# Optimization experiments

Measured on AMD Instinct MI355X. Metric: run time of the kernel, lower is better.

The kernel has to match this reference:

```python
import jax, jax.numpy as jnp
import numpy as np

D_MODEL = 1024
N_HEADS = 16
D_K = D_MODEL // N_HEADS
B, S = 4, 1024


def setup_inputs() -> dict:
    key = jax.random.key(0)
    ks = jax.random.split(key, 9)
    inp = {
        "q": jax.random.normal(ks[0], (B, S, D_MODEL), jnp.float32),
        "k": jax.random.normal(ks[1], (B, S, D_MODEL), jnp.float32),
        "v": jax.random.normal(ks[2], (B, S, D_MODEL), jnp.float32),
        # causal mask, broadcastable to [B, H, S, S]; 0 => masked
        "mask": jnp.tril(jnp.ones((1, 1, S, S), jnp.int32)),
        # torch nn.Linear weights: y = x @ W.T + b, W is [out, in]
        "Wq": jax.random.normal(ks[3], (D_MODEL, D_MODEL), jnp.float32) * 0.02,
        "bq": jnp.zeros((D_MODEL,), jnp.float32),
        "Wk": jax.random.normal(ks[4], (D_MODEL, D_MODEL), jnp.float32) * 0.02,
        "bk": jnp.zeros((D_MODEL,), jnp.float32),
        "Wv": jax.random.normal(ks[5], (D_MODEL, D_MODEL), jnp.float32) * 0.02,
        "bv": jnp.zeros((D_MODEL,), jnp.float32),
    }
    return inp


def _head_split(x):
    # [B, S, D] -> [B, H, S, d_k]
    b, s, _ = x.shape
    return x.reshape(b, s, N_HEADS, D_K).transpose(0, 2, 1, 3)


def reference(q, k, v, mask, Wq, bq, Wk, bk, Wv, bv):
    origin_shape = q.shape
    qh = _head_split(q @ Wq.T + bq)  # [B,H,S,dk]
    kh = _head_split(k @ Wk.T + bk)
    vh = _head_split(v @ Wv.T + bv)

    scores = jnp.einsum("bhqd,bhkd->bhqk", qh, kh) / jnp.sqrt(jnp.float32(D_K))
    scores = jnp.where(mask == 0, -jnp.inf, scores)
    # original subtracts the GLOBAL max before softmax (mathematically a no-op
    # per-row, kept for faithfulness)
    scores = jax.nn.softmax(scores - scores.max(), axis=-1)
    scores = jnp.where(jnp.isnan(scores), 0.0, scores)  # fully-masked rows -> 0

    out = jnp.einsum("bhqk,bhkd->bhqd", scores, vh)
    out = out.transpose(0, 2, 1, 3).reshape(origin_shape)
    return out, scores
```

## Files before the change

kernel.cpp:

```cpp
#include <hip/hip_runtime.h>

#define BATCH 4
#define SEQ 1024
#define DMODEL 1024
#define NH 16
#define DK 64

typedef float f32x4 __attribute__((ext_vector_type(4)));
typedef __bf16 bf16x8 __attribute__((ext_vector_type(8)));
typedef __bf16 bf16x4 __attribute__((ext_vector_type(4)));

#define MFMA(a, b, c) __builtin_amdgcn_mfma_f32_16x16x32_bf16((a), (b), (c), 0, 0, 0)

#define GLL16(g, l)                                                            \
    __builtin_amdgcn_global_load_lds(                                          \
        (const __attribute__((address_space(1))) void*)(g),                    \
        (__attribute__((address_space(3))) void*)(l), 16, 0, 0)

__global__ __launch_bounds__(256) void cvt6(
    const float* __restrict__ s0, const float* __restrict__ s1, const float* __restrict__ s2,
    const float* __restrict__ s3, const float* __restrict__ s4, const float* __restrict__ s5,
    __bf16* __restrict__ Xb, __bf16* __restrict__ Wb)
{
    const int z = blockIdx.z;
    const float* s = (z == 0) ? s0 : (z == 1) ? s1 : (z == 2) ? s2
                   : (z == 3) ? s3 : (z == 4) ? s4 : s5;
    __bf16* d = (z < 3) ? (Xb + (size_t)z * 4194304) : (Wb + (size_t)(z - 3) * 1048576);
    const int n = (z < 3) ? 4194304 : 1048576;

    const int idx = (blockIdx.x * 256 + threadIdx.x) * 8;
    if (idx < n) {
        const float4 lo = *(const float4*)(s + idx);
        const float4 hi = *(const float4*)(s + idx + 4);
        bf16x8 o;
        o[0] = (__bf16)lo.x; o[1] = (__bf16)lo.y; o[2] = (__bf16)lo.z; o[3] = (__bf16)lo.w;
        o[4] = (__bf16)hi.x; o[5] = (__bf16)hi.y; o[6] = (__bf16)hi.z; o[7] = (__bf16)hi.w;
        *(bf16x8*)(d + idx) = o;
    }
}

#define QKV_STAGE(dstA, dstB, k0)                                              \
    {                                                                          \
        GLL16(Xg + (size_t)(i0 +  0 + lane) * 2048 + (k0) * 2 + wid * 16,      \
              (dstA) + wid * 2048);                                            \
        GLL16(Xg + (size_t)(i0 + 64 + lane) * 2048 + (k0) * 2 + wid * 16,      \
              (dstA) + wid * 2048 + 1024);                                     \
        GLL16(Wg + (size_t)(j0 +  0 + lane) * 2048 + (k0) * 2 + wid * 16,      \
              (dstB) + wid * 2048);                                            \
        GLL16(Wg + (size_t)(j0 + 64 + lane) * 2048 + (k0) * 2 + wid * 16,      \
              (dstB) + wid * 2048 + 1024);                                     \
    }

__global__ __launch_bounds__(256, 2) void qkv_gemm(
    const __bf16* __restrict__ Xball, const __bf16* __restrict__ Wball,
    const float* __restrict__ bq, const float* __restrict__ bk, const float* __restrict__ bv,
    __bf16* __restrict__ qh, __bf16* __restrict__ kh, __bf16* __restrict__ vt)
{
    const int mat = blockIdx.z;
    const float* bias = (mat == 0) ? bq : (mat == 1) ? bk : bv;
    __bf16* dst       = (mat == 0) ? qh : (mat == 1) ? kh : vt;

    __shared__ __align__(16) __bf16 As[2][4096];
    __shared__ __align__(16) __bf16 Bs[2][4096];

    const int tid  = threadIdx.x;
    const int lane = tid & 63;
    const int wid  = tid >> 6;
    const int wr = wid >> 1, wc = wid & 1;
    const int lc = lane & 15, lg = lane >> 4;
    const int i0 = blockIdx.y * 128;
    const int j0 = blockIdx.x * 128;

    const char* Xg = (const char*)(Xball + (size_t)mat * 4096 * 1024);
    const char* Wg = (const char*)(Wball + (size_t)mat * 1024 * 1024);

    f32x4 acc[4][4] = {};

    QKV_STAGE((char*)&As[0][0], (char*)&Bs[0][0], 0);

    int cur = 0;
    for (int k0 = 0; k0 < DMODEL; k0 += 32, cur ^= 1) {
        if (k0 + 32 < DMODEL)
            QKV_STAGE((char*)&As[cur ^ 1][0], (char*)&Bs[cur ^ 1][0], k0 + 32);

        if (k0 + 32 < DMODEL) { asm volatile("s_waitcnt vmcnt(4)" ::: "memory"); }
        else                  { asm volatile("s_waitcnt vmcnt(0)" ::: "memory"); }
        __builtin_amdgcn_s_barrier();

        const char* ab = (const char*)&As[cur][0];
        const char* bb = (const char*)&Bs[cur][0];
        bf16x8 a[4], b[4];
        #pragma unroll
        for (int m = 0; m < 4; ++m)
            a[m] = *(const bf16x8*)(ab + lg * 2048 + (wr * 64 + m * 16 + lc) * 16);
        #pragma unroll
        for (int n = 0; n < 4; ++n)
            b[n] = *(const bf16x8*)(bb + lg * 2048 + (wc * 64 + n * 16 + lc) * 16);
        #pragma unroll
        for (int m = 0; m < 4; ++m)
            #pragma unroll
            for (int n = 0; n < 4; ++n)
                acc[m][n] = MFMA(a[m], b[n], acc[m][n]);

        asm volatile("s_waitcnt lgkmcnt(0)" ::: "memory");
        __builtin_amdgcn_s_barrier();
    }

    #pragma unroll
    for (int n = 0; n < 4; ++n) {
        const int j = j0 + wc * 64 + n * 16 + lc;
        const float bj = bias[j];
        const int h = j >> 6, d = j & 63;
        #pragma unroll
        for (int m = 0; m < 4; ++m) {
            #pragma unroll
            for (int r = 0; r < 4; ++r) {
                const int i = i0 + wr * 64 + m * 16 + lg * 4 + r;
                const int bb2 = i >> 10, s = i & 1023;
                const __bf16 o = (__bf16)(acc[m][n][r] + bj);
                if (mat < 2) dst[(((size_t)(bb2 * NH + h)) * SEQ + s) * DK + d] = o;
                else         dst[(((size_t)(bb2 * NH + h)) * DK + d) * SEQ + s] = o;
            }
        }
    }
}

#define STAGE_K(buf, kt)                                                       \
    {                                                                          \
        const char* gb_ = (const char*)Kb + (size_t)(kt) * 8192;               \
        char* lb_ = (char*)&Ks[buf][0];                                        \
        GLL16(gb_ + (wid * 2 + 0) * 1024 + soff, lb_ + (wid * 2 + 0) * 1024);  \
        GLL16(gb_ + (wid * 2 + 1) * 1024 + soff, lb_ + (wid * 2 + 1) * 1024);  \
    }

#define STAGE_V(kt)                                                            \
    {                                                                          \
        const char* gb_ = (const char*)Vb + (size_t)(kt) * 128;                \
        char* lb_ = (char*)&Vs[0];                                             \
        GLL16(gb_ + (size_t)((wid * 2 + 0) * 8 + sg) * 2048 + svoff,           \
              lb_ + (wid * 2 + 0) * 1024);                                     \
        GLL16(gb_ + (size_t)((wid * 2 + 1) * 8 + sg) * 2048 + svoff,           \
              lb_ + (wid * 2 + 1) * 1024);                                     \
    }

#define QK_TILE(kbuf, acc)                                                     \
    {                                                                          \
        const char* kb_ = (const char*)&Ks[kbuf][0];                           \
        _Pragma("unroll")                                                      \
        for (int n = 0; n < 4; ++n) {                                          \
            const int row_ = n * 16 + lc;                                      \
            const int sw_ = (row_ & 7) << 4;                                   \
            acc[n] = MFMA(aq0, *(const bf16x8*)(kb_ + row_ * 128 + ((lg * 16) ^ sw_)), acc[n]);      \
            acc[n] = MFMA(aq1, *(const bf16x8*)(kb_ + row_ * 128 + ((64 + lg * 16) ^ sw_)), acc[n]); \
        }                                                                      \
    }

__global__ __launch_bounds__(256, 4) void attn_fused9(
    const __bf16* __restrict__ qh, const __bf16* __restrict__ kh,
    const __bf16* __restrict__ vt, float* __restrict__ out, float* __restrict__ scores)
{
    const int id = blockIdx.x;
    const int bh = id & 63;
    const int g = id >> 6, h = g & 3, q = g >> 2;
    const int qb = (q & 1) ? (2 * h + (q >> 1)) : (15 - (q >> 1) - 2 * h);
    const int q0 = qb * 64;
    const int tid  = threadIdx.x;
    const int lane = tid & 63;
    const int wid  = tid >> 6;
    const int lc = lane & 15, lg = lane >> 4;
    const int r0 = wid * 16;

    __shared__ __align__(16) __bf16 Ks[2][64 * 64];
    __shared__ __align__(16) __bf16 Vs[64 * 64];
    __shared__ __align__(16) __bf16 Pf[4][16][72];

    const __bf16* Kb = kh + (size_t)bh * SEQ * DK;
    const __bf16* Vb = vt + (size_t)bh * DK * SEQ;

    const int sg    = lane >> 3;
    const int svoff = (((lane & 7) << 4)) ^ (sg << 4);
    const int soff  = (sg << 7) + svoff;

    float* srow = scores + ((size_t)bh * SEQ + q0 + r0) * SEQ;
    const int srr = lane >> 4;
    const int scc = (lane & 15) * 4;
    for (int kt = qb + 1; kt < 16; ++kt) {
        const f32x4 z = {};
        #pragma unroll
        for (int i = 0; i < 4; ++i)
            *(f32x4*)(srow + (size_t)(srr + 4 * i) * SEQ + kt * 64 + scc) = z;
    }

    const __bf16* Qp = qh + ((size_t)bh * SEQ + q0 + r0 + lc) * DK + lg * 8;
    const bf16x8 aq0 = *(const bf16x8*)(Qp);
    const bf16x8 aq1 = *(const bf16x8*)(Qp + 32);

    STAGE_K(0, 0);
    __syncthreads();

    float lsum[4] = {0.f, 0.f, 0.f, 0.f};
    for (int kt = 0; kt <= qb; ++kt) {
        if (kt < qb) STAGE_K((kt + 1) & 1, kt + 1);
        f32x4 acc[4] = {};
        QK_TILE(kt & 1, acc);
        if (kt < qb) {
            #pragma unroll
            for (int n = 0; n < 4; ++n)
                #pragma unroll
                for (int r = 0; r < 4; ++r)
                    lsum[r] += __expf(acc[n][r] * 0.125f);
        } else {
            #pragma unroll
            for (int n = 0; n < 4; ++n)
                #pragma unroll
                for (int r = 0; r < 4; ++r)
                    if (n * 16 + lc <= r0 + lg * 4 + r)
                        lsum[r] += __expf(acc[n][r] * 0.125f);
        }
        __syncthreads();
    }

    float linv[4];
    #pragma unroll
    for (int r = 0; r < 4; ++r) {
        float s = lsum[r];
        s += __shfl_xor(s, 1);
        s += __shfl_xor(s, 2);
        s += __shfl_xor(s, 4);
        s += __shfl_xor(s, 8);
        linv[r] = 1.0f / s;
    }

    STAGE_K(0, 0);
    f32x4 oacc[4] = {};
    __syncthreads();

    for (int kt = 0; kt <= qb; ++kt) {
        const int cur = kt & 1;
        STAGE_V(kt);
        if (kt < qb) STAGE_K(cur ^ 1, kt + 1);

        f32x4 acc[4] = {};
        QK_TILE(cur, acc);

        const bool diag = (kt == qb);
        float ps[4][4];
        #pragma unroll
        for (int n = 0; n < 4; ++n) {
            #pragma unroll
            for (int r = 0; r < 4; ++r) {
                float p = __expf(acc[n][r] * 0.125f) * linv[r];
                if (diag && (n * 16 + lc > r0 + lg * 4 + r)) p = 0.f;
                ps[n][r] = p;
                Pf[wid][lg * 4 + r][n * 16 + lc] = (__bf16)p;
            }
        }

        if (kt < qb) { asm volatile("s_waitcnt vmcnt(2)" ::: "memory"); }
        else         { asm volatile("s_waitcnt vmcnt(0)" ::: "memory"); }
        __builtin_amdgcn_s_barrier();

        {
            const char* vb_ = (const char*)&Vs[0];
            #pragma unroll
            for (int cc = 0; cc < 2; ++cc) {
                const bf16x8 pa = *(const bf16x8*)&Pf[wid][lc][cc * 32 + lg * 8];
                #pragma unroll
                for (int n = 0; n < 4; ++n) {
                    const int row_ = n * 16 + lc;
                    const int sw_ = (row_ & 7) << 4;
                    const bf16x8 vb = *(const bf16x8*)(vb_ + row_ * 128 + ((cc * 64 + lg * 16) ^ sw_));
                    oacc[n] = MFMA(pa, vb, oacc[n]);
                }
            }
        }

        {
            float* sp = srow + kt * 64;
            #pragma unroll
            for (int n = 0; n < 4; ++n)
                #pragma unroll
                for (int r = 0; r < 4; ++r)
                    sp[(size_t)(lg * 4 + r) * SEQ + n * 16 + lc] = ps[n][r];
        }

        asm volatile("s_waitcnt vmcnt(16)" ::: "memory");
        __builtin_amdgcn_s_barrier();
    }

    {
        const int b = bh >> 4, h2 = bh & 15;
        float* op = out + ((size_t)b * SEQ + q0 + r0) * DMODEL + h2 * DK;
        #pragma unroll
        for (int n = 0; n < 4; ++n)
            #pragma unroll
            for (int r = 0; r < 4; ++r)
                op[(size_t)(lg * 4 + r) * DMODEL + n * 16 + lc] = oacc[n][r];
    }
}

extern "C" void kernel_launch(void* const* d_in, const int* in_sizes, int n_in,
                              void* d_out, int out_size, void* d_ws, size_t ws_size,
                              hipStream_t stream)
{
    const float* q  = (const float*)d_in[0];
    const float* k  = (const float*)d_in[1];
    const float* v  = (const float*)d_in[2];
    const float* Wq = (const float*)d_in[4];
    const float* bq = (const float*)d_in[5];
    const float* Wk = (const float*)d_in[6];
    const float* bk = (const float*)d_in[7];
    const float* Wv = (const float*)d_in[8];
    const float* bv = (const float*)d_in[9];

    float* out    = (float*)d_out;
    float* scores = out + (size_t)BATCH * SEQ * DMODEL;

    __bf16* qh = (__bf16*)d_ws;
    __bf16* kh = qh + (size_t)BATCH * NH * SEQ * DK;
    __bf16* vt = kh + (size_t)BATCH * NH * SEQ * DK;

    __bf16* Xb = (__bf16*)scores;
    __bf16* Wb = Xb + (size_t)3 * 4096 * 1024;

    cvt6<<<dim3(2048, 1, 6), 256, 0, stream>>>(q, k, v, Wq, Wk, Wv, Xb, Wb);

    dim3 g1(DMODEL / 128, (BATCH * SEQ) / 128, 3);
    qkv_gemm<<<g1, 256, 0, stream>>>(Xb, Wb, bq, bk, bv, qh, kh, vt);

    attn_fused9<<<dim3(16 * 64), 256, 0, stream>>>(qh, kh, vt, out, scores);
}
```

Measured before the change: 148.1 us.

## Double QKV GEMM k-tile to 64 with XOR-swizzled row-major LDS layout

The QKV projection GEMM now stages a 64-wide K slice per iteration instead of 32. This halves the number of barrier and wait rounds in the main loop. The LDS tile changes from a k-chunk-major layout to a row-major layout of 128 bytes per row, with a 16-byte chunk XOR swizzle on row&7 so that the fragment reads avoid bank conflicts. LDS use per block doubles to 64 KB, which could limit the two-blocks-per-CU occupancy target, and each wave now issues more global-to-LDS loads per stage.

New measurement: 139.5 us, median of 2. 1.06x faster.

```diff
diff --git a/kernel.cpp b/kernel.cpp
--- a/kernel.cpp
+++ b/kernel.cpp
@@ -39,16 +39,16 @@
     }
 }
 
-#define QKV_STAGE(dstA, dstB, k0)                                              \
+#define QKV_STAGE64(dstA, dstB, k0)                                            \
     {                                                                          \
-        GLL16(Xg + (size_t)(i0 +  0 + lane) * 2048 + (k0) * 2 + wid * 16,      \
-              (dstA) + wid * 2048);                                            \
-        GLL16(Xg + (size_t)(i0 + 64 + lane) * 2048 + (k0) * 2 + wid * 16,      \
-              (dstA) + wid * 2048 + 1024);                                     \
-        GLL16(Wg + (size_t)(j0 +  0 + lane) * 2048 + (k0) * 2 + wid * 16,      \
-              (dstB) + wid * 2048);                                            \
-        GLL16(Wg + (size_t)(j0 + 64 + lane) * 2048 + (k0) * 2 + wid * 16,      \
-              (dstB) + wid * 2048 + 1024);                                     \
+        _Pragma("unroll")                                                      \
+        for (int q_ = 0; q_ < 4; ++q_) {                                       \
+            const int r8_ = wid * 32 + q_ * 8;   \
+            GLL16(Xg + (size_t)(i0 + r8_ + rsub) * 2048 + (k0) * 2 + schk * 16,\
+                  (dstA) + r8_ * 128);                                         \
+            GLL16(Wg + (size_t)(j0 + r8_ + rsub) * 2048 + (k0) * 2 + schk * 16,\
+                  (dstB) + r8_ * 128);                                         \
+        }                                                                      \
     }
 
 __global__ __launch_bounds__(256, 2) void qkv_gemm(
@@ -60,8 +60,8 @@
     const float* bias = (mat == 0) ? bq : (mat == 1) ? bk : bv;
     __bf16* dst       = (mat == 0) ? qh : (mat == 1) ? kh : vt;
 
-    __shared__ __align__(16) __bf16 As[2][4096];
-    __shared__ __align__(16) __bf16 Bs[2][4096];
+    __shared__ __align__(16) __bf16 As[2][8192];
+    __shared__ __align__(16) __bf16 Bs[2][8192];
 
     const int tid  = threadIdx.x;
     const int lane = tid & 63;
@@ -71,36 +71,46 @@
     const int i0 = blockIdx.y * 128;
     const int j0 = blockIdx.x * 128;
 
+    const int rsub = lane >> 3;
+    const int schk = (lane & 7) ^ rsub;
+
     const char* Xg = (const char*)(Xball + (size_t)mat * 4096 * 1024);
     const char* Wg = (const char*)(Wball + (size_t)mat * 1024 * 1024);
 
     f32x4 acc[4][4] = {};
 
-    QKV_STAGE((char*)&As[0][0], (char*)&Bs[0][0], 0);
+    QKV_STAGE64((char*)&As[0][0], (char*)&Bs[0][0], 0);
 
     int cur = 0;
-    for (int k0 = 0; k0 < DMODEL; k0 += 32, cur ^= 1) {
-        if (k0 + 32 < DMODEL)
-            QKV_STAGE((char*)&As[cur ^ 1][0], (char*)&Bs[cur ^ 1][0], k0 + 32);
-
-        if (k0 + 32 < DMODEL) { asm volatile("s_waitcnt vmcnt(4)" ::: "memory"); }
+    for (int k0 = 0; k0 < DMODEL; k0 += 64, cur ^= 1) {
+        if (k0 + 64 < DMODEL)
+            QKV_STAGE64((char*)&As[cur ^ 1][0], (char*)&Bs[cur ^ 1][0], k0 + 64);
+
+        if (k0 + 64 < DMODEL) { asm volatile("s_waitcnt vmcnt(8)" ::: "memory"); }
         else                  { asm volatile("s_waitcnt vmcnt(0)" ::: "memory"); }
         __builtin_amdgcn_s_barrier();
 
         const char* ab = (const char*)&As[cur][0];
         const char* bb = (const char*)&Bs[cur][0];
-        bf16x8 a[4], b[4];
-        #pragma unroll
-        for (int m = 0; m < 4; ++m)
-            a[m] = *(const bf16x8*)(ab + lg * 2048 + (wr * 64 + m * 16 + lc) * 16);
-        #pragma unroll
-        for (int n = 0; n < 4; ++n)
-            b[n] = *(const bf16x8*)(bb + lg * 2048 + (wc * 64 + n * 16 + lc) * 16);
-        #pragma unroll
-        for (int m = 0; m < 4; ++m)
-            #pragma unroll
-            for (int n = 0; n < 4; ++n)
-                acc[m][n] = MFMA(a[m], b[n], acc[m][n]);
+        #pragma unroll
+        for (int kk = 0; kk < 2; ++kk) {
+            bf16x8 a[4], b[4];
+            #pragma unroll
+            for (int m = 0; m < 4; ++m) {
+                const int row = wr * 64 + m * 16 + lc;
+                a[m] = *(const bf16x8*)(ab + row * 128 + (((kk * 4 + lg) ^ (row & 7)) * 16));
+            }
+            #pragma unroll
+            for (int n = 0; n < 4; ++n) {
+                const int row = wc * 64 + n * 16 + lc;
+                b[n] = *(const bf16x8*)(bb + row * 128 + (((kk * 4 + lg) ^ (row & 7)) * 16));
+            }
+            #pragma unroll
+            for (int m = 0; m < 4; ++m)
+                #pragma unroll
+                for (int n = 0; n < 4; ++n)
+                    acc[m][n] = MFMA(a[m], b[n], acc[m][n]);
+        }
 
         asm volatile("s_waitcnt lgkmcnt(0)" ::: "memory");
         __builtin_amdgcn_s_barrier();
```
